# Performance work log

Measured on AMD Instinct MI355X. Metric: run time of the kernel, lower is better.

## Reference

```python
import jax, jax.numpy as jnp
import numpy as np

B, S, E, H = 4, 1024, 1024, 16
D = E // H
LN_EPS = 1e-5
W_SCALE = 0.02  # keep pre-softmax scores positive and moderate


def _linear(x, W, b):
    return x @ W + b


def _layernorm(x, g, b):
    m = jnp.mean(x, axis=-1, keepdims=True)
    v = jnp.mean((x - m) ** 2, axis=-1, keepdims=True)
    return (x - m) * jax.lax.rsqrt(v + LN_EPS) * g + b


def setup_inputs() -> dict:
    key = jax.random.key(0)
    ks = jax.random.split(key, 24)
    u = lambda k, shape, s=1.0: jax.random.uniform(k, shape, dtype=jnp.float32) * s
    inp = {
        'value': u(ks[0], (B, S, E)),
        'key':   u(ks[1], (B, S, E)),
        'query': u(ks[2], (B, S, E)),
        'mask':  jnp.ones((B, 1, 1, S), dtype=jnp.int32),
        # attention projections (W stored as [in, out])
        'Wv': u(ks[3], (E, E), W_SCALE), 'bv': u(ks[4], (E,), W_SCALE),
        'Wk': u(ks[5], (E, E), W_SCALE), 'bk': u(ks[6], (E,), W_SCALE),
        'Wq': u(ks[7], (E, E), W_SCALE), 'bq': u(ks[8], (E,), W_SCALE),
        'Wo': u(ks[9], (E, E), W_SCALE), 'bo': u(ks[10], (E,), W_SCALE),
        # feed-forward
        'W1': u(ks[11], (E, 4 * E), W_SCALE), 'b1': u(ks[12], (4 * E,), W_SCALE),
        'W2': u(ks[13], (4 * E, E), W_SCALE), 'b2': u(ks[14], (E,), W_SCALE),
        # layer norms
        'g1': jnp.ones((E,), jnp.float32), 'be1': jnp.zeros((E,), jnp.float32),
        'g2': jnp.ones((E,), jnp.float32), 'be2': jnp.zeros((E,), jnp.float32),
    }
    return inp


def reference(value, key, query, mask, Wv, bv, Wk, bk, Wq, bq, Wo, bo,
              W1, b1, W2, b2, g1, be1, g2, be2):
    b, q_len, _ = query.shape
    v = _linear(value, Wv, bv).reshape(b, -1, H, D)   # [B,K,H,D]
    k = _linear(key, Wk, bk).reshape(b, -1, H, D)     # [B,K,H,D]
    q = _linear(query, Wq, bq).reshape(b, q_len, H, D)
    att = jnp.einsum('bqhd,bkhd->bhqk', q, k)         # raw scores
    att = jnp.where(mask == 0, -jnp.inf, att)
    att = jnp.power(att, -0.5)                        # custom score^{-1/2} transform
    att = jax.nn.softmax(att, axis=3)
    ctx = jnp.einsum('bhqk,bkhd->bqhd', att, v).reshape(b, q_len, E)
    attn_out = _linear(ctx, Wo, bo)
    x = _layernorm(attn_out + query, g1, be1)         # dropout = identity (eval)
    ff = _linear(jax.nn.relu(_linear(x, W1, b1)), W2, b2)
    return _layernorm(ff + x, g2, be2)
```

## Files before the change

kernel.cpp:

```cpp
#include <hip/hip_runtime.h>
#include <hip/hip_bf16.h>
#include <cstdint>

typedef __hip_bfloat16 bf16;
typedef float f32x4 __attribute__((ext_vector_type(4)));
typedef short bf16x8 __attribute__((ext_vector_type(8)));
typedef short bf16x4v __attribute__((ext_vector_type(4)));

#define S_LEN 1024
#define EDIM  1024

__device__ __forceinline__ float bfs2f(short s) {
  return __uint_as_float(((unsigned)(unsigned short)s) << 16);
}
__device__ __forceinline__ short f2bfs(float f) {
  union { __hip_bfloat16 h; short s; } u;
  u.h = __float2bfloat16(f);
  return u.s;
}
__device__ __forceinline__ void glds16(const void* g, void* l) {
  __builtin_amdgcn_global_load_lds(
      (const __attribute__((address_space(1))) void*)g,
      (__attribute__((address_space(3))) void*)l, 16, 0, 0);
}
__device__ __forceinline__ float score_xform(float s) {
  float r, e;
  asm("v_rsq_f32 %0, %1" : "=v"(r) : "v"(s));
  r *= 1.44269504088896f;
  asm("v_exp_f32 %0, %1" : "=v"(e) : "v"(r));
  return e;
}
__device__ __forceinline__ int xcd_swz(int bid, int nwg) {
  const int q = nwg >> 3, r = nwg & 7, xcd = bid & 7, j = bid >> 3;
  return (xcd < r ? xcd * (q + 1) : r * (q + 1) + (xcd - r) * q) + j;
}
#define BAR() do { __builtin_amdgcn_s_barrier(); asm volatile("" ::: "memory"); } while (0)
#define WAITV(n) asm volatile("s_waitcnt vmcnt(" #n ")" ::: "memory")

struct Cvt3 { const float* in[3]; bf16* out[3]; };
__global__ __launch_bounds__(256)
void k_cvt3(Cvt3 p, int n4) {
  const float4* in = (const float4*)p.in[blockIdx.y];
  bf16x4v* out = (bf16x4v*)p.out[blockIdx.y];
  for (int i = blockIdx.x * 256 + threadIdx.x; i < n4; i += gridDim.x * 256) {
    float4 v = in[i];
    bf16x4v o;
    o[0] = f2bfs(v.x); o[1] = f2bfs(v.y); o[2] = f2bfs(v.z); o[3] = f2bfs(v.w);
    out[i] = o;
  }
}

struct TW4 { const float* in[4]; bf16* out[4]; };
__global__ void k_transpose_w4(TW4 p) {
  __shared__ bf16 t[32][33];
  const float* in = p.in[blockIdx.z];
  bf16* out = p.out[blockIdx.z];
  const int c0 = blockIdx.x * 32, r0 = blockIdx.y * 32;
  const int x = threadIdx.x;
  for (int yy = threadIdx.y; yy < 32; yy += 8)
    t[yy][x] = __float2bfloat16(in[(size_t)(r0 + yy) * 1024 + c0 + x]);
  __syncthreads();
  for (int yy = threadIdx.y; yy < 32; yy += 8)
    out[(size_t)(c0 + yy) * 1024 + r0 + x] = t[x][yy];
}

__global__ void k_transpose_w(const float* __restrict__ in, bf16* __restrict__ out,
                              int R, int C) {
  __shared__ bf16 t[32][33];
  const int c0 = blockIdx.x * 32, r0 = blockIdx.y * 32;
  const int x = threadIdx.x;
  for (int yy = threadIdx.y; yy < 32; yy += 8)
    t[yy][x] = __float2bfloat16(in[(size_t)(r0 + yy) * C + c0 + x]);
  __syncthreads();
  for (int yy = threadIdx.y; yy < 32; yy += 8)
    out[(size_t)(c0 + yy) * R + r0 + x] = t[x][yy];
}

__global__ void k_transpose_v(const bf16* __restrict__ v, bf16* __restrict__ vt) {
  __shared__ bf16 t[32][33];
  const int bh = blockIdx.z;
  const bf16* in = v + (size_t)(bh >> 4) * S_LEN * EDIM + (bh & 15) * 64;
  bf16* out = vt + (size_t)bh * 64 * S_LEN;
  const int d0 = blockIdx.x * 32, s0 = blockIdx.y * 32;
  const int x = threadIdx.x;
  for (int yy = threadIdx.y; yy < 32; yy += 8)
    t[yy][x] = in[(size_t)(s0 + yy) * EDIM + d0 + x];
  __syncthreads();
  for (int yy = threadIdx.y; yy < 32; yy += 8)
    out[(size_t)(d0 + yy) * S_LEN + s0 + x] = t[x][yy];
}

template <int RELU, int OUT_F32, int HAS_BIAS>
__device__ __forceinline__ void gemm8_body(
    const bf16* __restrict__ A, int lda, const bf16* __restrict__ Bt, int ldb,
    const float* __restrict__ bias, void* __restrict__ Cout, int ldc,
    int K, int koff, int bm, int bn, char* smem) {
  const int tid = threadIdx.x, lane = tid & 63, wid = tid >> 6;
  const int wm = wid >> 2;
  const int wn = wid & 3;
  const int fr = lane & 15, fg = lane >> 4;
  const int sw = (fr & 7) << 4;

  const int rr = lane >> 3;
  const int cc = ((lane & 7) ^ rr) << 3;

  #define STG(src, ld, dstoff)                                                  \
    {                                                                           \
      const bf16* _s = (src);                                                   \
      _Pragma("unroll")                                                         \
      for (int _j = 0; _j < 2; _j++) {                                          \
        const int _L = wid * 2 + _j;                                            \
        glds16(_s + (size_t)(_L * 8 + rr) * (ld) + cc, smem + (dstoff) + _L * 1024); \
      }                                                                         \
    }

  const bf16* Abase = A + (size_t)bm * lda + koff;
  const bf16* Bbase = Bt + (size_t)bn * ldb + koff;
  const int nt = K >> 6;

  STG(Abase + cc * 0, lda, 0);
  STG(Abase + (size_t)128 * lda, lda, 16384);
  STG(Bbase, ldb, 32768);
  STG(Bbase + (size_t)128 * ldb, ldb, 49152);
  if (nt > 1) {
    STG(Bbase + 64, ldb, 65536 + 32768);
    STG(Bbase + (size_t)128 * ldb + 64, ldb, 65536 + 49152);
  }
  WAITV(0);
  BAR();

  f32x4 acc[8][4] = {};
  bf16x8 af[4][2], b01[2][2], b23[2][2];

  const int aRd = wm * 16384 + fr * 128;
  const int bRd = 32768 + (wn >> 1) * 16384 + (wn & 1) * 8192 + fr * 128;
  const int c0s = (0 * 64 + fg * 16) ^ sw;
  const int c1s = (1 * 64 + fg * 16) ^ sw;

  for (int n = 0; n < nt; n++) {
    const int buf = (n & 1) << 16;
    const int nbuf = buf ^ 65536;
    const char* sb = smem + buf;
    const int kA = (n + 1) << 6;
    const int kB = (n + 2) << 6;

#pragma unroll
    for (int i = 0; i < 4; i++) {
      af[i][0] = *(const bf16x8*)(sb + aRd + i * 2048 + c0s);
      af[i][1] = *(const bf16x8*)(sb + aRd + i * 2048 + c1s);
    }
#pragma unroll
    for (int j = 0; j < 2; j++) {
      b01[j][0] = *(const bf16x8*)(sb + bRd + j * 2048 + c0s);
      b01[j][1] = *(const bf16x8*)(sb + bRd + j * 2048 + c1s);
    }
    if (n + 1 < nt) STG(Abase + kA, lda, nbuf);
    BAR();
    __builtin_amdgcn_s_setprio(1);
#pragma unroll
    for (int i = 0; i < 4; i++)
#pragma unroll
      for (int j = 0; j < 2; j++) {
        acc[i][j] = __builtin_amdgcn_mfma_f32_16x16x32_bf16(af[i][0], b01[j][0], acc[i][j], 0, 0, 0);
        acc[i][j] = __builtin_amdgcn_mfma_f32_16x16x32_bf16(af[i][1], b01[j][1], acc[i][j], 0, 0, 0);
      }
    __builtin_amdgcn_s_setprio(0);
    BAR();

#pragma unroll
    for (int j = 0; j < 2; j++) {
      b23[j][0] = *(const bf16x8*)(sb + bRd + (j + 2) * 2048 + c0s);
      b23[j][1] = *(const bf16x8*)(sb + bRd + (j + 2) * 2048 + c1s);
    }
    if (n + 1 < nt) STG(Abase + (size_t)128 * lda + kA, lda, nbuf + 16384);
    BAR();
    __builtin_amdgcn_s_setprio(1);
#pragma unroll
    for (int i = 0; i < 4; i++)
#pragma unroll
      for (int j = 0; j < 2; j++) {
        acc[i][j + 2] = __builtin_amdgcn_mfma_f32_16x16x32_bf16(af[i][0], b23[j][0], acc[i][j + 2], 0, 0, 0);
        acc[i][j + 2] = __builtin_amdgcn_mfma_f32_16x16x32_bf16(af[i][1], b23[j][1], acc[i][j + 2], 0, 0, 0);
      }
    __builtin_amdgcn_s_setprio(0);
    BAR();

#pragma unroll
    for (int i = 0; i < 4; i++) {
      af[i][0] = *(const bf16x8*)(sb + aRd + (i + 4) * 2048 + c0s);
      af[i][1] = *(const bf16x8*)(sb + aRd + (i + 4) * 2048 + c1s);
    }
    if (n + 2 < nt) STG(Bbase + kB, ldb, buf + 32768);
    BAR();
    __builtin_amdgcn_s_setprio(1);
#pragma unroll
    for (int i = 0; i < 4; i++)
#pragma unroll
      for (int j = 0; j < 2; j++) {
        acc[i + 4][j + 2] = __builtin_amdgcn_mfma_f32_16x16x32_bf16(af[i][0], b23[j][0], acc[i + 4][j + 2], 0, 0, 0);
        acc[i + 4][j + 2] = __builtin_amdgcn_mfma_f32_16x16x32_bf16(af[i][1], b23[j][1], acc[i + 4][j + 2], 0, 0, 0);
      }
    __builtin_amdgcn_s_setprio(0);
    BAR();

    if (n + 2 < nt) STG(Bbase + (size_t)128 * ldb + kB, ldb, buf + 49152);
    __builtin_amdgcn_s_setprio(1);
#pragma unroll
    for (int i = 0; i < 4; i++)
#pragma unroll
      for (int j = 0; j < 2; j++) {
        acc[i + 4][j] = __builtin_amdgcn_mfma_f32_16x16x32_bf16(af[i][0], b01[j][0], acc[i + 4][j], 0, 0, 0);
        acc[i + 4][j] = __builtin_amdgcn_mfma_f32_16x16x32_bf16(af[i][1], b01[j][1], acc[i + 4][j], 0, 0, 0);
      }
    __builtin_amdgcn_s_setprio(0);
    if (n + 2 < nt) { WAITV(4); } else { WAITV(0); }
    BAR();
  }
  #undef STG

  float bv4[4];
#pragma unroll
  for (int j = 0; j < 4; j++)
    bv4[j] = HAS_BIAS ? bias[bn + wn * 64 + j * 16 + fr] : 0.f;
#pragma unroll
  for (int i = 0; i < 8; i++) {
    const size_t rowb = (size_t)bm + wm * 128 + i * 16 + fg * 4;
#pragma unroll
    for (int r = 0; r < 4; r++) {
#pragma unroll
      for (int j = 0; j < 4; j++) {
        float v = acc[i][j][r] + bv4[j];
        if (RELU) v = fmaxf(v, 0.f);
        const size_t idx = (rowb + r) * (size_t)ldc + bn + wn * 64 + j * 16 + fr;
        if (OUT_F32) ((float*)Cout)[idx] = v;
        else ((bf16*)Cout)[idx] = __float2bfloat16(v);
      }
    }
  }
}

struct G8Args {
  const bf16* A; int lda; const bf16* Bt; int ldb; const float* bias;
  void* C[4]; int ldc; int Kz;
};
template <int RELU, int OUT_F32, int HAS_BIAS>
__global__ __launch_bounds__(512, 2)
void k_gemm8(G8Args a) {
  __shared__ __align__(16) char smem[131072];
  const int nwg = gridDim.x * gridDim.y;
  const int bid = xcd_swz(blockIdx.y * gridDim.x + blockIdx.x, nwg);
  const int bx = bid % gridDim.x, by = bid / gridDim.x;
  gemm8_body<RELU, OUT_F32, HAS_BIAS>(
      a.A, a.lda, a.Bt, a.ldb, a.bias, a.C[blockIdx.z], a.ldc,
      a.Kz, blockIdx.z * a.Kz, by * 256, bx * 256, smem);
}

struct QkvArgs { const bf16* A[3]; const bf16* B[3]; const float* bias[3]; bf16* C[3]; };
__global__ __launch_bounds__(512, 2)
void k_gemm8_qkv(QkvArgs p) {
  __shared__ __align__(16) char smem[131072];
  const int nwg = gridDim.x * gridDim.y;
  const int bid = xcd_swz(blockIdx.y * gridDim.x + blockIdx.x, nwg);
  const int bx = bid % (int)gridDim.x;
  int by = bid / (int)gridDim.x;
  const int grp = by >> 4;
  by &= 15;
  gemm8_body<0, 0, 1>(p.A[grp], 1024, p.B[grp], 1024, p.bias[grp],
                      (void*)p.C[grp], 1024, 1024, 0, by * 256, bx * 256, smem);
}

__global__ __launch_bounds__(256)
void k_attn(const bf16* __restrict__ q, const bf16* __restrict__ k,
            const bf16* __restrict__ vt, bf16* __restrict__ ctx) {
  const int qt = blockIdx.x;
  const int bh = blockIdx.y;
  const int b = bh >> 4, h = bh & 15;
  const int tid = threadIdx.x, lane = tid & 63, w = tid >> 6;
  const int fr = lane & 15, fg = lane >> 4;
  const bf16* Q  = q  + (size_t)b * S_LEN * EDIM + h * 64;
  const bf16* Kp = k  + (size_t)b * S_LEN * EDIM + h * 64;
  const bf16* V  = vt + (size_t)bh * 64 * S_LEN;

  __shared__ __align__(16) bf16 lK[2][64 * 64];
  __shared__ __align__(16) bf16 lV[2][64 * 64];
  __shared__ __align__(16) bf16 eL[4][32][72];

  const int srow = lane >> 3;
  const int scol = (((lane & 7) ^ srow) << 3);
  const int rsw  = (fr & 7) << 3;

  bf16x8 qf[2][2];
#pragma unroll
  for (int i = 0; i < 2; i++)
#pragma unroll
    for (int ks = 0; ks < 2; ks++)
      qf[i][ks] = *(const bf16x8*)(Q + (size_t)(qt * 128 + w * 32 + i * 16 + fr) * EDIM + ks * 32 + fg * 8);

#pragma unroll
  for (int c = 0; c < 2; c++) {
    const int r = w * 8 + c * 32 + srow;
    glds16(Kp + (size_t)r * EDIM + scol, (char*)&lK[0][(w * 8 + c * 32) * 64]);
    glds16(V + (size_t)r * S_LEN + scol, (char*)&lV[0][(w * 8 + c * 32) * 64]);
  }
  __syncthreads();

  f32x4 accO[2][4] = {};
  float lsum[2][4] = {};
  int cur = 0;
  for (int kt = 0; kt < S_LEN; kt += 64) {
    if (kt + 64 < S_LEN) {
#pragma unroll
      for (int c = 0; c < 2; c++) {
        const int r = w * 8 + c * 32 + srow;
        glds16(Kp + (size_t)(kt + 64 + r) * EDIM + scol,
               (char*)&lK[cur ^ 1][(w * 8 + c * 32) * 64]);
        glds16(V + (size_t)r * S_LEN + kt + 64 + scol,
               (char*)&lV[cur ^ 1][(w * 8 + c * 32) * 64]);
      }
    }
    f32x4 accS[2][4] = {};
#pragma unroll
    for (int ks = 0; ks < 2; ks++)
#pragma unroll
      for (int j = 0; j < 4; j++) {
        bf16x8 kf = *(const bf16x8*)(&lK[cur][(j * 16 + fr) * 64 + ((ks * 32 + fg * 8) ^ rsw)]);
#pragma unroll
        for (int i = 0; i < 2; i++)
          accS[i][j] = __builtin_amdgcn_mfma_f32_16x16x32_bf16(qf[i][ks], kf, accS[i][j], 0, 0, 0);
      }
#pragma unroll
    for (int i = 0; i < 2; i++)
#pragma unroll
      for (int j = 0; j < 4; j++)
#pragma unroll
        for (int r = 0; r < 4; r++) {
          float p = score_xform(accS[i][j][r]);
          lsum[i][r] += p;
          eL[w][i * 16 + fg * 4 + r][j * 16 + fr] = __float2bfloat16(p);
        }
#pragma unroll
    for (int ks = 0; ks < 2; ks++) {
      bf16x8 af[2];
#pragma unroll
      for (int i = 0; i < 2; i++)
        af[i] = *(const bf16x8*)(&eL[w][i * 16 + fr][ks * 32 + fg * 8]);
#pragma unroll
      for (int j = 0; j < 4; j++) {
        bf16x8 vf = *(const bf16x8*)(&lV[cur][(j * 16 + fr) * 64 + ((ks * 32 + fg * 8) ^ rsw)]);
#pragma unroll
        for (int i = 0; i < 2; i++)
          accO[i][j] = __builtin_amdgcn_mfma_f32_16x16x32_bf16(af[i], vf, accO[i][j], 0, 0, 0);
      }
    }
    __syncthreads();
    cur ^= 1;
  }

#pragma unroll
  for (int i = 0; i < 2; i++)
#pragma unroll
    for (int r = 0; r < 4; r++) {
      float s = lsum[i][r];
      s += __shfl_xor(s, 1, 64);
      s += __shfl_xor(s, 2, 64);
      s += __shfl_xor(s, 4, 64);
      s += __shfl_xor(s, 8, 64);
      lsum[i][r] = s;
    }
#pragma unroll
  for (int i = 0; i < 2; i++)
#pragma unroll
    for (int r = 0; r < 4; r++) {
      const size_t qrow = (size_t)qt * 128 + w * 32 + i * 16 + fg * 4 + r;
      const float inv = 1.0f / lsum[i][r];
#pragma unroll
      for (int j = 0; j < 4; j++)
        ctx[((size_t)b * S_LEN + qrow) * EDIM + h * 64 + j * 16 + fr] =
            __float2bfloat16(accO[i][j][r] * inv);
    }
}

struct LnP { const float* p[4]; };
template <int NP, int RES_F32, int OUT_F32>
__global__ __launch_bounds__(256)
void k_ln_resN(LnP pp, const float* __restrict__ bias, const void* res_,
               const float* __restrict__ g, const float* __restrict__ be,
               void* out_) {
  const int row = blockIdx.x;
  const int tid = threadIdx.x;
  const int lane = tid & 63, wid = tid >> 6;
  const size_t base = (size_t)row * EDIM + tid * 4;
  float4 c = *(const float4*)(bias + tid * 4);
  float x[4] = {c.x, c.y, c.z, c.w};
#pragma unroll
  for (int t = 0; t < NP; t++) {
    float4 v = *(const float4*)(pp.p[t] + base);
    x[0] += v.x; x[1] += v.y; x[2] += v.z; x[3] += v.w;
  }
  if (RES_F32) {
    float4 v = *(const float4*)((const float*)res_ + base);
    x[0] += v.x; x[1] += v.y; x[2] += v.z; x[3] += v.w;
  } else {
    bf16x4v v = *(const bf16x4v*)((const bf16*)res_ + base);
#pragma unroll
    for (int i = 0; i < 4; i++) x[i] += bfs2f(v[i]);
  }

  float s = x[0] + x[1] + x[2] + x[3];
#pragma unroll
  for (int o = 32; o >= 1; o >>= 1) s += __shfl_xor(s, o, 64);
  __shared__ float red[4], red2[4];
  if (lane == 0) red[wid] = s;
  __syncthreads();
  const float mean = (red[0] + red[1] + red[2] + red[3]) * (1.0f / 1024.0f);

  float d[4], s2 = 0.f;
#pragma unroll
  for (int i = 0; i < 4; i++) { d[i] = x[i] - mean; s2 += d[i] * d[i]; }
#pragma unroll
  for (int o = 32; o >= 1; o >>= 1) s2 += __shfl_xor(s2, o, 64);
  if (lane == 0) red2[wid] = s2;
  __syncthreads();
  const float var = (red2[0] + red2[1] + red2[2] + red2[3]) * (1.0f / 1024.0f);
  const float inv = rsqrtf(var + 1e-5f);

  float4 g4 = *(const float4*)(g + tid * 4);
  float4 b4 = *(const float4*)(be + tid * 4);
  float o0 = d[0] * inv * g4.x + b4.x;
  float o1 = d[1] * inv * g4.y + b4.y;
  float o2 = d[2] * inv * g4.z + b4.z;
  float o3 = d[3] * inv * g4.w + b4.w;
  if (OUT_F32) {
    *(float4*)((float*)out_ + base) = make_float4(o0, o1, o2, o3);
  } else {
    bf16x4v o;
    o[0] = f2bfs(o0); o[1] = f2bfs(o1); o[2] = f2bfs(o2); o[3] = f2bfs(o3);
    *(bf16x4v*)((bf16*)out_ + base) = o;
  }
}

extern "C" void kernel_launch(void* const* d_in, const int* in_sizes, int n_in,
                              void* d_out, int out_size, void* d_ws, size_t ws_size,
                              hipStream_t stream) {
  const float* value = (const float*)d_in[0];
  const float* key_  = (const float*)d_in[1];
  const float* query = (const float*)d_in[2];
  const float* Wv = (const float*)d_in[4];  const float* bv = (const float*)d_in[5];
  const float* Wk = (const float*)d_in[6];  const float* bk = (const float*)d_in[7];
  const float* Wq = (const float*)d_in[8];  const float* bq = (const float*)d_in[9];
  const float* Wo = (const float*)d_in[10]; const float* bo = (const float*)d_in[11];
  const float* W1 = (const float*)d_in[12]; const float* b1 = (const float*)d_in[13];
  const float* W2 = (const float*)d_in[14]; const float* b2 = (const float*)d_in[15];
  const float* g1 = (const float*)d_in[16]; const float* be1 = (const float*)d_in[17];
  const float* g2 = (const float*)d_in[18]; const float* be2 = (const float*)d_in[19];

  char* wsb = (char*)d_ws;
  const size_t MB = 1024 * 1024;
  bf16* W1T = (bf16*)(wsb + 0 * MB);
  bf16* W2T = (bf16*)(wsb + 8 * MB);
  bf16* WqT = (bf16*)(wsb + 16 * MB);
  bf16* WkT = (bf16*)(wsb + 18 * MB);
  bf16* WvT = (bf16*)(wsb + 20 * MB);
  bf16* WoT = (bf16*)(wsb + 22 * MB);
  bf16* qx  = (bf16*)(wsb + 24 * MB);
  bf16* kx  = (bf16*)(wsb + 32 * MB);
  bf16* vx  = (bf16*)(wsb + 40 * MB);
  bf16* qb  = (bf16*)(wsb + 48 * MB);
  bf16* kb  = (bf16*)(wsb + 56 * MB);
  bf16* vb  = (bf16*)(wsb + 64 * MB);
  bf16* vtb = (bf16*)(wsb + 72 * MB);
  bf16* ctx = (bf16*)(wsb + 24 * MB);
  float* p0w = (float*)(wsb + 32 * MB);
  float* p1w = (float*)(wsb + 48 * MB);
  bf16* xb  = (bf16*)(wsb + 16 * MB);
  bf16* h1  = (bf16*)(wsb + 24 * MB);
  float* f1 = (float*)(wsb + 56 * MB);
  float* f2 = (float*)(wsb + 72 * MB);
  float* f3 = (float*)(wsb + 88 * MB);
  const int splitF = (ws_size >= 108 * MB) ? 4 : 2;

  const dim3 tb(32, 8);
  Cvt3 cp;
  cp.in[0] = query; cp.out[0] = qx;
  cp.in[1] = key_;  cp.out[1] = kx;
  cp.in[2] = value; cp.out[2] = vx;
  k_cvt3<<<dim3(1024, 3), 256, 0, stream>>>(cp, 1024 * 1024);

  TW4 tw;
  tw.in[0] = Wq; tw.out[0] = WqT;
  tw.in[1] = Wk; tw.out[1] = WkT;
  tw.in[2] = Wv; tw.out[2] = WvT;
  tw.in[3] = Wo; tw.out[3] = WoT;
  k_transpose_w4<<<dim3(32, 32, 4), tb, 0, stream>>>(tw);
  k_transpose_w<<<dim3(128, 32), tb, 0, stream>>>(W1, W1T, 1024, 4096);
  k_transpose_w<<<dim3(32, 128), tb, 0, stream>>>(W2, W2T, 4096, 1024);

  QkvArgs qp;
  qp.A[0] = qx; qp.B[0] = WqT; qp.bias[0] = bq; qp.C[0] = qb;
  qp.A[1] = kx; qp.B[1] = WkT; qp.bias[1] = bk; qp.C[1] = kb;
  qp.A[2] = vx; qp.B[2] = WvT; qp.bias[2] = bv; qp.C[2] = vb;
  k_gemm8_qkv<<<dim3(4, 48), 512, 0, stream>>>(qp);

  k_transpose_v<<<dim3(2, 32, 64), tb, 0, stream>>>(vb, vtb);
  k_attn<<<dim3(8, 64), 256, 0, stream>>>(qb, kb, vtb, ctx);

  G8Args wo;
  wo.A = ctx; wo.lda = 1024; wo.Bt = WoT; wo.ldb = 1024; wo.bias = nullptr;
  wo.C[0] = p0w; wo.C[1] = p1w; wo.C[2] = nullptr; wo.C[3] = nullptr;
  wo.ldc = 1024; wo.Kz = 512;
  k_gemm8<0, 1, 0><<<dim3(4, 16, 2), 512, 0, stream>>>(wo);
  LnP l1; l1.p[0] = p0w; l1.p[1] = p1w; l1.p[2] = nullptr; l1.p[3] = nullptr;
  k_ln_resN<2, 1, 0><<<4096, 256, 0, stream>>>(l1, bo, query, g1, be1, xb);

  G8Args ff1;
  ff1.A = xb; ff1.lda = 1024; ff1.Bt = W1T; ff1.ldb = 1024; ff1.bias = b1;
  ff1.C[0] = h1; ff1.C[1] = nullptr; ff1.C[2] = nullptr; ff1.C[3] = nullptr;
  ff1.ldc = 4096; ff1.Kz = 1024;
  k_gemm8<1, 0, 1><<<dim3(16, 16, 1), 512, 0, stream>>>(ff1);

  G8Args ff2;
  ff2.A = h1; ff2.lda = 4096; ff2.Bt = W2T; ff2.ldb = 4096; ff2.bias = nullptr;
  ff2.C[0] = d_out; ff2.C[1] = f1; ff2.C[2] = f2; ff2.C[3] = f3;
  ff2.ldc = 1024; ff2.Kz = 4096 / splitF;
  k_gemm8<0, 1, 0><<<dim3(4, 16, splitF), 512, 0, stream>>>(ff2);

  LnP l2;
  l2.p[0] = (const float*)d_out; l2.p[1] = f1; l2.p[2] = f2; l2.p[3] = f3;
  if (splitF == 4)
    k_ln_resN<4, 0, 1><<<4096, 256, 0, stream>>>(l2, b2, xb, g2, be2, (float*)d_out);
  else
    k_ln_resN<2, 0, 1><<<4096, 256, 0, stream>>>(l2, b2, xb, g2, be2, (float*)d_out);
}
```

Baseline: 233.3 us.

## Fuse weight transposes, rebalance split-K for Wo and FF2, reorder attention grid

Merges all six weight transpose launches into one kernel, and generalises the GEMM split-K to per-slice K offsets and lengths. The Wo projection becomes a three-way uneven split-K, and FF2 gains a three-way option for mid-sized workspaces. The attention grid is reordered so head index varies fastest. The aim is fewer launches and better CU occupancy for the small GEMMs, at the cost of an extra fp32 partial buffer to write and reduce in the layernorm.

```diff
diff --git a/kernel.cpp b/kernel.cpp
--- a/kernel.cpp
+++ b/kernel.cpp
@@ -50,30 +50,23 @@
   }
 }
 
-struct TW4 { const float* in[4]; bf16* out[4]; };
-__global__ void k_transpose_w4(TW4 p) {
-  __shared__ bf16 t[32][33];
-  const float* in = p.in[blockIdx.z];
-  bf16* out = p.out[blockIdx.z];
-  const int c0 = blockIdx.x * 32, r0 = blockIdx.y * 32;
+struct TAll { const float* in[6]; bf16* out[6]; };
+__global__ void k_transpose_all(TAll p) {
+  int t = blockIdx.x;
+  int z, tr, tc, R, C;
+  if (t < 4096)      { z = t >> 10; R = 1024; C = 1024; int i = t & 1023; tr = i >> 5; tc = i & 31; }
+  else if (t < 8192) { z = 4; R = 1024; C = 4096; int i = t - 4096; tr = i >> 7; tc = i & 127; }
+  else               { z = 5; R = 4096; C = 1024; int i = t - 8192; tr = i >> 5; tc = i & 31; }
+  __shared__ bf16 tile[32][33];
+  const float* in = p.in[z];
+  bf16* out = p.out[z];
+  const int c0 = tc * 32, r0 = tr * 32;
   const int x = threadIdx.x;
   for (int yy = threadIdx.y; yy < 32; yy += 8)
-    t[yy][x] = __float2bfloat16(in[(size_t)(r0 + yy) * 1024 + c0 + x]);
+    tile[yy][x] = __float2bfloat16(in[(size_t)(r0 + yy) * C + c0 + x]);
   __syncthreads();
   for (int yy = threadIdx.y; yy < 32; yy += 8)
-    out[(size_t)(c0 + yy) * 1024 + r0 + x] = t[x][yy];
-}
-
-__global__ void k_transpose_w(const float* __restrict__ in, bf16* __restrict__ out,
-                              int R, int C) {
-  __shared__ bf16 t[32][33];
-  const int c0 = blockIdx.x * 32, r0 = blockIdx.y * 32;
-  const int x = threadIdx.x;
-  for (int yy = threadIdx.y; yy < 32; yy += 8)
-    t[yy][x] = __float2bfloat16(in[(size_t)(r0 + yy) * C + c0 + x]);
-  __syncthreads();
-  for (int yy = threadIdx.y; yy < 32; yy += 8)
-    out[(size_t)(c0 + yy) * R + r0 + x] = t[x][yy];
+    out[(size_t)(c0 + yy) * R + r0 + x] = tile[x][yy];
 }
 
 __global__ void k_transpose_v(const bf16* __restrict__ v, bf16* __restrict__ vt) {
@@ -118,7 +111,7 @@
   const bf16* Bbase = Bt + (size_t)bn * ldb + koff;
   const int nt = K >> 6;
 
-  STG(Abase + cc * 0, lda, 0);
+  STG(Abase, lda, 0);
   STG(Abase + (size_t)128 * lda, lda, 16384);
   STG(Bbase, ldb, 32768);
   STG(Bbase + (size_t)128 * ldb, ldb, 49152);
@@ -241,7 +234,7 @@
 
 struct G8Args {
   const bf16* A; int lda; const bf16* Bt; int ldb; const float* bias;
-  void* C[4]; int ldc; int Kz;
+  void* C[4]; int ldc; int koffz[4]; int Kzz[4];
 };
 template <int RELU, int OUT_F32, int HAS_BIAS>
 __global__ __launch_bounds__(512, 2)
@@ -250,9 +243,10 @@
   const int nwg = gridDim.x * gridDim.y;
   const int bid = xcd_swz(blockIdx.y * gridDim.x + blockIdx.x, nwg);
   const int bx = bid % gridDim.x, by = bid / gridDim.x;
+  const int z = blockIdx.z;
   gemm8_body<RELU, OUT_F32, HAS_BIAS>(
-      a.A, a.lda, a.Bt, a.ldb, a.bias, a.C[blockIdx.z], a.ldc,
-      a.Kz, blockIdx.z * a.Kz, by * 256, bx * 256, smem);
+      a.A, a.lda, a.Bt, a.ldb, a.bias, a.C[z], a.ldc,
+      a.Kzz[z], a.koffz[z], by * 256, bx * 256, smem);
 }
 
 struct QkvArgs { const bf16* A[3]; const bf16* B[3]; const float* bias[3]; bf16* C[3]; };
@@ -272,8 +266,8 @@
 __global__ __launch_bounds__(256)
 void k_attn(const bf16* __restrict__ q, const bf16* __restrict__ k,
             const bf16* __restrict__ vt, bf16* __restrict__ ctx) {
-  const int qt = blockIdx.x;
-  const int bh = blockIdx.y;
+  const int bh = blockIdx.x;
+  const int qt = blockIdx.y;
   const int b = bh >> 4, h = bh & 15;
   const int tid = threadIdx.x, lane = tid & 63, w = tid >> 6;
   const int fr = lane & 15, fg = lane >> 4;
@@ -472,12 +466,13 @@
   bf16* ctx = (bf16*)(wsb + 24 * MB);
   float* p0w = (float*)(wsb + 32 * MB);
   float* p1w = (float*)(wsb + 48 * MB);
+  float* p2w = (float*)(wsb + 64 * MB);
   bf16* xb  = (bf16*)(wsb + 16 * MB);
   bf16* h1  = (bf16*)(wsb + 24 * MB);
   float* f1 = (float*)(wsb + 56 * MB);
   float* f2 = (float*)(wsb + 72 * MB);
   float* f3 = (float*)(wsb + 88 * MB);
-  const int splitF = (ws_size >= 108 * MB) ? 4 : 2;
+  const int splitF = (ws_size >= 104 * MB) ? 4 : (ws_size >= 88 * MB) ? 3 : 2;
 
   const dim3 tb(32, 8);
   Cvt3 cp;
@@ -486,14 +481,14 @@
   cp.in[2] = value; cp.out[2] = vx;
   k_cvt3<<<dim3(1024, 3), 256, 0, stream>>>(cp, 1024 * 1024);
 
-  TW4 tw;
-  tw.in[0] = Wq; tw.out[0] = WqT;
-  tw.in[1] = Wk; tw.out[1] = WkT;
-  tw.in[2] = Wv; tw.out[2] = WvT;
-  tw.in[3] = Wo; tw.out[3] = WoT;
-  k_transpose_w4<<<dim3(32, 32, 4), tb, 0, stream>>>(tw);
-  k_transpose_w<<<dim3(128, 32), tb, 0, stream>>>(W1, W1T, 1024, 4096);
-  k_transpose_w<<<dim3(32, 128), tb, 0, stream>>>(W2, W2T, 4096, 1024);
+  TAll ta;
+  ta.in[0] = Wq; ta.out[0] = WqT;
+  ta.in[1] = Wk; ta.out[1] = WkT;
+  ta.in[2] = Wv; ta.out[2] = WvT;
+  ta.in[3] = Wo; ta.out[3] = WoT;
+  ta.in[4] = W1; ta.out[4] = W1T;
+  ta.in[5] = W2; ta.out[5] = W2T;
+  k_transpose_all<<<12288, tb, 0, stream>>>(ta);
 
   QkvArgs qp;
   qp.A[0] = qx; qp.B[0] = WqT; qp.bias[0] = bq; qp.C[0] = qb;
@@ -502,32 +497,55 @@
   k_gemm8_qkv<<<dim3(4, 48), 512, 0, stream>>>(qp);
 
   k_transpose_v<<<dim3(2, 32, 64), tb, 0, stream>>>(vb, vtb);
-  k_attn<<<dim3(8, 64), 256, 0, stream>>>(qb, kb, vtb, ctx);
+  k_attn<<<dim3(64, 8), 256, 0, stream>>>(qb, kb, vtb, ctx);
 
   G8Args wo;
   wo.A = ctx; wo.lda = 1024; wo.Bt = WoT; wo.ldb = 1024; wo.bias = nullptr;
-  wo.C[0] = p0w; wo.C[1] = p1w; wo.C[2] = nullptr; wo.C[3] = nullptr;
-  wo.ldc = 1024; wo.Kz = 512;
-  k_gemm8<0, 1, 0><<<dim3(4, 16, 2), 512, 0, stream>>>(wo);
-  LnP l1; l1.p[0] = p0w; l1.p[1] = p1w; l1.p[2] = nullptr; l1.p[3] = nullptr;
-  k_ln_resN<2, 1, 0><<<4096, 256, 0, stream>>>(l1, bo, query, g1, be1, xb);
+  wo.C[0] = p0w; wo.C[1] = p1w; wo.C[2] = p2w; wo.C[3] = nullptr;
+  wo.ldc = 1024;
+  wo.koffz[0] = 0;   wo.Kzz[0] = 384;
+  wo.koffz[1] = 384; wo.Kzz[1] = 320;
+  wo.koffz[2] = 704; wo.Kzz[2] = 320;
+  wo.koffz[3] = 0;   wo.Kzz[3] = 64;
+  k_gemm8<0, 1, 0><<<dim3(4, 16, 3), 512, 0, stream>>>(wo);
+  LnP l1; l1.p[0] = p0w; l1.p[1] = p1w; l1.p[2] = p2w; l1.p[3] = nullptr;
+  k_ln_resN<3, 1, 0><<<4096, 256, 0, stream>>>(l1, bo, query, g1, be1, xb);
 
   G8Args ff1;
   ff1.A = xb; ff1.lda = 1024; ff1.Bt = W1T; ff1.ldb = 1024; ff1.bias = b1;
   ff1.C[0] = h1; ff1.C[1] = nullptr; ff1.C[2] = nullptr; ff1.C[3] = nullptr;
-  ff1.ldc = 4096; ff1.Kz = 1024;
+  ff1.ldc = 4096;
+  ff1.koffz[0] = 0; ff1.Kzz[0] = 1024;
+  ff1.koffz[1] = 0; ff1.Kzz[1] = 64;
+  ff1.koffz[2] = 0; ff1.Kzz[2] = 64;
+  ff1.koffz[3] = 0; ff1.Kzz[3] = 64;
   k_gemm8<1, 0, 1><<<dim3(16, 16, 1), 512, 0, stream>>>(ff1);
 
   G8Args ff2;
   ff2.A = h1; ff2.lda = 4096; ff2.Bt = W2T; ff2.ldb = 4096; ff2.bias = nullptr;
   ff2.C[0] = d_out; ff2.C[1] = f1; ff2.C[2] = f2; ff2.C[3] = f3;
-  ff2.ldc = 1024; ff2.Kz = 4096 / splitF;
+  ff2.ldc = 1024;
+  if (splitF == 4) {
+    for (int z = 0; z < 4; z++) { ff2.koffz[z] = z * 1024; ff2.Kzz[z] = 1024; }
+  } else if (splitF == 3) {
+    ff2.koffz[0] = 0;    ff2.Kzz[0] = 1344;
+    ff2.koffz[1] = 1344; ff2.Kzz[1] = 1344;
+    ff2.koffz[2] = 2688; ff2.Kzz[2] = 1408;
+    ff2.koffz[3] = 0;    ff2.Kzz[3] = 64;
+  } else {
+    ff2.koffz[0] = 0;    ff2.Kzz[0] = 2048;
+    ff2.koffz[1] = 2048; ff2.Kzz[1] = 2048;
+    ff2.koffz[2] = 0;    ff2.Kzz[2] = 64;
+    ff2.koffz[3] = 0;    ff2.Kzz[3] = 64;
+  }
   k_gemm8<0, 1, 0><<<dim3(4, 16, splitF), 512, 0, stream>>>(ff2);
 
   LnP l2;
   l2.p[0] = (const float*)d_out; l2.p[1] = f1; l2.p[2] = f2; l2.p[3] = f3;
   if (splitF == 4)
     k_ln_resN<4, 0, 1><<<4096, 256, 0, stream>>>(l2, b2, xb, g2, be2, (float*)d_out);
+  else if (splitF == 3)
+    k_ln_resN<3, 0, 1><<<4096, 256, 0, stream>>>(l2, b2, xb, g2, be2, (float*)d_out);
   else
     k_ln_resN<2, 0, 1><<<4096, 256, 0, stream>>>(l2, b2, xb, g2, be2, (float*)d_out);
 }
```

Result: faster. 223.5 us (-4.2%).
